# Performance work log

Measured on AMD Instinct MI355X. Metric: run time of the kernel, lower is better.

## Reference

```python
import jax, jax.numpy as jnp
import numpy as np

NUM_HEADS = 16


def setup_inputs() -> dict:
    key = jax.random.key(0)
    k1, k2, k3 = jax.random.split(key, 3)
    B, N, C = 8, 1024, 1024
    x = jax.random.normal(k1, (B, N, C), dtype=jnp.float32)
    w_qkv = jax.random.normal(k2, (3 * C, C), dtype=jnp.float32) * (C ** -0.5)
    w_proj = jax.random.normal(k3, (C, C), dtype=jnp.float32) * (C ** -0.5)
    b_proj = jnp.zeros((C,), dtype=jnp.float32)
    return {"x": x, "w_qkv": w_qkv, "w_proj": w_proj, "b_proj": b_proj}


def reference(x, w_qkv, w_proj, b_proj):
    B, N, C = x.shape
    H = NUM_HEADS
    d = C // H
    scale = d ** -0.5
    # qkv projection: (B, N, 3C) -> (3, B, H, N, d)
    qkv = jnp.einsum('bnc,oc->bno', x, w_qkv)
    qkv = qkv.reshape(B, N, 3, H, d).transpose(2, 0, 3, 1, 4)
    q, k, v = qkv[0], qkv[1], qkv[2]
    # spatial attention
    attn = jnp.einsum('bhnd,bhmd->bhnm', q, k) * scale
    attn = jax.nn.softmax(attn, axis=-1)
    out = jnp.einsum('bhnm,bhmd->bhnd', attn, v)
    out = out.transpose(0, 2, 1, 3).reshape(B, N, C)
    # output projection
    return jnp.einsum('bnc,oc->bno', out, w_proj) + b_proj
```

## Files before the change

kernel.cpp:

```cpp
#include <hip/hip_runtime.h>
#include <hip/hip_bf16.h>

typedef unsigned short u16;
typedef unsigned int u32;
typedef __bf16 bf16x8 __attribute__((ext_vector_type(8)));
typedef float f32x4 __attribute__((ext_vector_type(4)));

__device__ __forceinline__ u16 f2b(float f) {
    __bf16 h = (__bf16)f;
    return __builtin_bit_cast(u16, h);
}
__device__ __forceinline__ u32 f2b2(float lo, float hi) {
    return (u32)f2b(lo) | ((u32)f2b(hi) << 16);
}
__device__ __forceinline__ f32x4 mfma16(bf16x8 a, bf16x8 b, f32x4 c) {
    return __builtin_amdgcn_mfma_f32_16x16x32_bf16(a, b, c, 0, 0, 0);
}
__device__ __forceinline__ void async16(const u16* gsrc, u16* ldst) {
    __builtin_amdgcn_global_load_lds(
        (const __attribute__((address_space(1))) void*)gsrc,
        (__attribute__((address_space(3))) void*)ldst, 16, 0, 0);
}

__global__ __launch_bounds__(256) void cvt_all(const float* __restrict__ x,
                                               const float* __restrict__ wq,
                                               const float* __restrict__ wp,
                                               u16* __restrict__ xb,
                                               u16* __restrict__ wqb,
                                               u16* __restrict__ wpb) {
    int i = (blockIdx.x * 256 + threadIdx.x) * 4;
    const float* src; u16* dst; int off;
    if (i < 8388608)       { src = x;  dst = xb;  off = i; }
    else if (i < 11534336) { src = wq; dst = wqb; off = i - 8388608; }
    else                   { src = wp; dst = wpb; off = i - 11534336; }
    float4 f = *(const float4*)(src + off);
    ushort4 o;
    o.x = f2b(f.x); o.y = f2b(f.y); o.z = f2b(f.z); o.w = f2b(f.w);
    *(ushort4*)(dst + off) = o;
}

template <bool F32OUT>
__device__ __forceinline__ void gemm_core(const u16* __restrict__ A,
                                          const u16* __restrict__ B,
                                          void* __restrict__ Cptr,
                                          const float* __restrict__ bias,
                                          int N, int K, int bm, int bn,
                                          u16* As, u16* Bs) {
    const int tid  = threadIdx.x;
    const int lane = tid & 63, wid = tid >> 6;
    const int quad = lane >> 4, l16 = lane & 15;
    const int wm = (wid >> 1) * 64, wn = (wid & 1) * 64;
    const int srow = tid >> 2;
    const int scol = (tid & 3) * 8;

    const u16* Abase = A + (size_t)(bm * 128) * K + scol;
    const u16* Bbase = B + (size_t)(bn * 128) * K + scol;

    f32x4 acc[4][4] = {};

    for (int k0 = 0; k0 < K; k0 += 32) {
        __syncthreads();
        async16(Abase + (size_t)srow * K + k0,        &As[wid * 512]);
        async16(Abase + (size_t)(64 + srow) * K + k0, &As[2048 + wid * 512]);
        async16(Bbase + (size_t)srow * K + k0,        &Bs[wid * 512]);
        async16(Bbase + (size_t)(64 + srow) * K + k0, &Bs[2048 + wid * 512]);
        __syncthreads();
        bf16x8 af[4], bfr[4];
#pragma unroll
        for (int mt = 0; mt < 4; mt++)
            af[mt] = *(const bf16x8*)&As[(wm + mt * 16 + l16) * 32 + quad * 8];
#pragma unroll
        for (int nt = 0; nt < 4; nt++)
            bfr[nt] = *(const bf16x8*)&Bs[(wn + nt * 16 + l16) * 32 + quad * 8];
#pragma unroll
        for (int mt = 0; mt < 4; mt++)
#pragma unroll
            for (int nt = 0; nt < 4; nt++)
                acc[mt][nt] = mfma16(af[mt], bfr[nt], acc[mt][nt]);
    }
#pragma unroll
    for (int mt = 0; mt < 4; mt++) {
#pragma unroll
        for (int nt = 0; nt < 4; nt++) {
            int row = bm * 128 + wm + mt * 16 + quad * 4;
            int col = bn * 128 + wn + nt * 16 + l16;
            float bv = F32OUT ? bias[col] : 0.f;
#pragma unroll
            for (int r = 0; r < 4; r++) {
                if (F32OUT)
                    ((float*)Cptr)[(size_t)(row + r) * N + col] = acc[mt][nt][r] + bv;
                else
                    ((u16*)Cptr)[(size_t)(row + r) * N + col] = f2b(acc[mt][nt][r]);
            }
        }
    }
}

__global__ __launch_bounds__(256) void gemm_qkvt(const u16* __restrict__ xb,
                                                 const u16* __restrict__ wqkvb,
                                                 u16* __restrict__ qkb,
                                                 u16* __restrict__ vTb) {
    __shared__ u16 As[128 * 32];
    __shared__ u16 Bs[128 * 32];
    int id = blockIdx.x;
    if (id < 1024) {
        gemm_core<false>(xb, wqkvb, qkb, nullptr, 2048, 1024, id >> 4, id & 15, As, Bs);
    } else {
        int t = id - 1024;
        gemm_core<false>(wqkvb + (size_t)2048 * 1024, xb, vTb, nullptr,
                         8192, 1024, t >> 6, t & 63, As, Bs);
    }
}

__global__ __launch_bounds__(256) void gemm_proj(const u16* __restrict__ A,
                                                 const u16* __restrict__ B,
                                                 void* __restrict__ C,
                                                 const float* __restrict__ bias) {
    __shared__ u16 As[128 * 32];
    __shared__ u16 Bs[128 * 32];
    gemm_core<true>(A, B, C, bias, 1024, 1024, blockIdx.y, blockIdx.x, As, Bs);
}

__global__ __launch_bounds__(256, 4) void attn_kernel(const u16* __restrict__ qk,
                                                      const u16* __restrict__ vT,
                                                      u16* __restrict__ outb) {
    __shared__ u16 Qs[64 * 64];
    __shared__ u16 Ks[64 * 64];
    __shared__ u16 Vt[64 * 64];
    __shared__ u16 Ps[4 * 16 * 72];
    const int tid = threadIdx.x, lane = tid & 63, wid = tid >> 6;
    const int quad = lane >> 4, l16 = lane & 15;
    const int qt = blockIdx.x;
    const int bh = blockIdx.y;
    const int b = bh >> 4, h = bh & 15;
    const size_t base = (size_t)b * 1024;
    const int hoff = h * 64;
    const float CEXP = 0.125f * 1.44269504f;

    const int sr_ = lane >> 3;
    const int sc_ = ((lane & 7) ^ sr_) * 8;
    const int sw = l16 & 7;

#pragma unroll
    for (int j = 0; j < 2; ++j) {
        int rg = wid * 16 + j * 8;
        async16(qk + (base + qt * 64 + rg + sr_) * 2048 + hoff + sc_, &Qs[rg * 64]);
    }

    f32x4 Oacc[4] = {};
    float lp[4] = {0.f, 0.f, 0.f, 0.f};
    bf16x8 bq[2];
    u16* Pw = &Ps[wid * (16 * 72)];

    for (int kt = 0; kt < 16; ++kt) {
        __syncthreads();
#pragma unroll
        for (int j = 0; j < 2; ++j) {
            int rg = wid * 16 + j * 8;
            async16(qk + (base + kt * 64 + rg + sr_) * 2048 + 1024 + hoff + sc_,
                    &Ks[rg * 64]);
            async16(vT + (size_t)(hoff + rg + sr_) * 8192 + base + kt * 64 + sc_,
                    &Vt[rg * 64]);
        }
        __syncthreads();

        if (kt == 0) {
            int row = wid * 16 + l16;
            bq[0] = *(const bf16x8*)&Qs[row * 64 + ((quad ^ sw) << 3)];
            bq[1] = *(const bf16x8*)&Qs[row * 64 + (((4 + quad) ^ sw) << 3)];
        }

        f32x4 sacc[4] = {};
#pragma unroll
        for (int nt = 0; nt < 4; nt++) {
            int row = nt * 16 + l16;
            bf16x8 ak0 = *(const bf16x8*)&Ks[row * 64 + ((quad ^ sw) << 3)];
            bf16x8 ak1 = *(const bf16x8*)&Ks[row * 64 + (((4 + quad) ^ sw) << 3)];
            sacc[nt] = mfma16(ak0, bq[0], sacc[nt]);
            sacc[nt] = mfma16(ak1, bq[1], sacc[nt]);
        }

#pragma unroll
        for (int nt = 0; nt < 4; nt++) {
            float p0 = exp2f(sacc[nt][0] * CEXP);
            float p1 = exp2f(sacc[nt][1] * CEXP);
            float p2 = exp2f(sacc[nt][2] * CEXP);
            float p3 = exp2f(sacc[nt][3] * CEXP);
            lp[0] += p0; lp[1] += p1; lp[2] += p2; lp[3] += p3;
            uint2 pk; pk.x = f2b2(p0, p1); pk.y = f2b2(p2, p3);
            *(uint2*)&Pw[l16 * 72 + nt * 16 + quad * 4] = pk;
        }

        asm volatile("s_waitcnt lgkmcnt(0)" ::: "memory");
        __builtin_amdgcn_wave_barrier();

#pragma unroll
        for (int kc = 0; kc < 2; kc++) {
            bf16x8 ap = *(const bf16x8*)&Pw[l16 * 72 + kc * 32 + quad * 8];
#pragma unroll
            for (int nv = 0; nv < 4; nv++) {
                int row = nv * 16 + l16;
                bf16x8 bv = *(const bf16x8*)&Vt[row * 64 + (((kc * 4 + quad) ^ sw) << 3)];
                Oacc[nv] = mfma16(ap, bv, Oacc[nv]);
            }
        }
    }

    float l = (lp[0] + lp[1]) + (lp[2] + lp[3]);
    l += __shfl_xor(l, 16);
    l += __shfl_xor(l, 32);
    float inv[4];
#pragma unroll
    for (int r = 0; r < 4; r++) inv[r] = 1.f / __shfl(l, quad * 4 + r);

#pragma unroll
    for (int nv = 0; nv < 4; nv++)
#pragma unroll
        for (int r = 0; r < 4; r++) {
            int row = qt * 64 + wid * 16 + quad * 4 + r;
            int col = hoff + nv * 16 + l16;
            outb[(base + row) * 1024 + col] = f2b(Oacc[nv][r] * inv[r]);
        }
}

extern "C" void kernel_launch(void* const* d_in, const int* in_sizes, int n_in,
                              void* d_out, int out_size, void* d_ws, size_t ws_size,
                              hipStream_t stream) {
    const float* x      = (const float*)d_in[0];
    const float* w_qkv  = (const float*)d_in[1];
    const float* w_proj = (const float*)d_in[2];
    const float* b_proj = (const float*)d_in[3];

    char* ws = (char*)d_ws;
    u16* xb     = (u16*)(ws);
    u16* wqkvb  = (u16*)(ws + 16777216);
    u16* wprojb = (u16*)(ws + 23068672);
    u16* qkb    = (u16*)(ws + 25165824);
    u16* vTb    = (u16*)(ws + 58720256);
    u16* attnb  = (u16*)(ws + 75497472);

    cvt_all<<<12288, 256, 0, stream>>>(x, w_qkv, w_proj, xb, wqkvb, wprojb);
    gemm_qkvt<<<1536, 256, 0, stream>>>(xb, wqkvb, qkb, vTb);
    attn_kernel<<<dim3(16, 128), 256, 0, stream>>>(qkb, vTb, attnb);
    gemm_proj<<<dim3(8, 64), 256, 0, stream>>>(attnb, wprojb, d_out, b_proj);
}
```

Measured before the change: 252.5 us.

## Double-buffer K/V tiles in attention, fold softmax scale into Q weights

The attention kernel now double-buffers K and V tiles in LDS, prefetching the next tile while computing the current one, so each iteration needs one load-wait instead of a full load-then-compute serialization. Q is loaded straight from global into registers, dropping the Q LDS stage. The softmax scale times log2(e) is folded into the Q rows of the bf16 weight conversion, removing a multiply per score. Row sums are computed with an extra MFMA against a ones vector instead of per-lane adds and shuffles, and the P buffer uses an XOR swizzle rather than padding. Folding the scale into bf16 weights slightly changes rounding, and softmax still has no max subtraction.

```diff
diff --git a/kernel.cpp b/kernel.cpp
--- a/kernel.cpp
+++ b/kernel.cpp
@@ -29,13 +29,15 @@
                                                u16* __restrict__ wqb,
                                                u16* __restrict__ wpb) {
     int i = (blockIdx.x * 256 + threadIdx.x) * 4;
-    const float* src; u16* dst; int off;
-    if (i < 8388608)       { src = x;  dst = xb;  off = i; }
-    else if (i < 11534336) { src = wq; dst = wqb; off = i - 8388608; }
-    else                   { src = wp; dst = wpb; off = i - 11534336; }
+    const float* src; u16* dst; int off; float scl;
+    if (i < 8388608)       { src = x;  dst = xb;  off = i;            scl = 1.f; }
+    else if (i < 9437184)  { src = wq; dst = wqb; off = i - 8388608;  scl = 0.18033688f; }
+    else if (i < 11534336) { src = wq; dst = wqb; off = i - 8388608;  scl = 1.f; }
+    else                   { src = wp; dst = wpb; off = i - 11534336; scl = 1.f; }
     float4 f = *(const float4*)(src + off);
     ushort4 o;
-    o.x = f2b(f.x); o.y = f2b(f.y); o.z = f2b(f.z); o.w = f2b(f.w);
+    o.x = f2b(f.x * scl); o.y = f2b(f.y * scl);
+    o.z = f2b(f.z * scl); o.w = f2b(f.w * scl);
     *(ushort4*)(dst + off) = o;
 }
 
@@ -124,10 +126,9 @@
 __global__ __launch_bounds__(256, 4) void attn_kernel(const u16* __restrict__ qk,
                                                       const u16* __restrict__ vT,
                                                       u16* __restrict__ outb) {
-    __shared__ u16 Qs[64 * 64];
-    __shared__ u16 Ks[64 * 64];
-    __shared__ u16 Vt[64 * 64];
-    __shared__ u16 Ps[4 * 16 * 72];
+    __shared__ u16 Ks[2][64 * 64];
+    __shared__ u16 Vt[2][64 * 64];
+    __shared__ u16 Ps[4 * 16 * 64];
     const int tid = threadIdx.x, lane = tid & 63, wid = tid >> 6;
     const int quad = lane >> 4, l16 = lane & 15;
     const int qt = blockIdx.x;
@@ -135,83 +136,87 @@
     const int b = bh >> 4, h = bh & 15;
     const size_t base = (size_t)b * 1024;
     const int hoff = h * 64;
-    const float CEXP = 0.125f * 1.44269504f;
 
     const int sr_ = lane >> 3;
     const int sc_ = ((lane & 7) ^ sr_) * 8;
     const int sw = l16 & 7;
 
-#pragma unroll
-    for (int j = 0; j < 2; ++j) {
-        int rg = wid * 16 + j * 8;
-        async16(qk + (base + qt * 64 + rg + sr_) * 2048 + hoff + sc_, &Qs[rg * 64]);
-    }
-
-    f32x4 Oacc[4] = {};
-    float lp[4] = {0.f, 0.f, 0.f, 0.f};
-    bf16x8 bq[2];
-    u16* Pw = &Ps[wid * (16 * 72)];
-
-    for (int kt = 0; kt < 16; ++kt) {
-        __syncthreads();
+    const u16* qptr = qk + (base + qt * 64 + wid * 16 + l16) * 2048 + hoff + quad * 8;
+    bf16x8 bq0 = *(const bf16x8*)qptr;
+    bf16x8 bq1 = *(const bf16x8*)(qptr + 32);
+
+    auto stage = [&](int kt, int bs) {
 #pragma unroll
         for (int j = 0; j < 2; ++j) {
             int rg = wid * 16 + j * 8;
             async16(qk + (base + kt * 64 + rg + sr_) * 2048 + 1024 + hoff + sc_,
-                    &Ks[rg * 64]);
+                    &Ks[bs][rg * 64]);
             async16(vT + (size_t)(hoff + rg + sr_) * 8192 + base + kt * 64 + sc_,
-                    &Vt[rg * 64]);
-        }
-        __syncthreads();
-
-        if (kt == 0) {
-            int row = wid * 16 + l16;
-            bq[0] = *(const bf16x8*)&Qs[row * 64 + ((quad ^ sw) << 3)];
-            bq[1] = *(const bf16x8*)&Qs[row * 64 + (((4 + quad) ^ sw) << 3)];
-        }
+                    &Vt[bs][rg * 64]);
+        }
+    };
+    stage(0, 0);
+
+    f32x4 Oacc[4] = {};
+    f32x4 lacc = {};
+    bf16x8 vone;
+#pragma unroll
+    for (int i = 0; i < 8; ++i) vone[i] = (__bf16)1.0f;
+    u16* Pw = &Ps[wid * (16 * 64)];
+
+    for (int t = 0; t < 16; ++t) {
+        const int cur = t & 1;
+        __builtin_amdgcn_s_barrier();
+        __builtin_amdgcn_sched_barrier(0);
+        if (t < 15) {
+            stage(t + 1, cur ^ 1);
+            asm volatile("s_waitcnt vmcnt(4)" ::: "memory");
+        } else {
+            asm volatile("s_waitcnt vmcnt(0)" ::: "memory");
+        }
+        __builtin_amdgcn_s_barrier();
+        __builtin_amdgcn_sched_barrier(0);
 
         f32x4 sacc[4] = {};
 #pragma unroll
         for (int nt = 0; nt < 4; nt++) {
             int row = nt * 16 + l16;
-            bf16x8 ak0 = *(const bf16x8*)&Ks[row * 64 + ((quad ^ sw) << 3)];
-            bf16x8 ak1 = *(const bf16x8*)&Ks[row * 64 + (((4 + quad) ^ sw) << 3)];
-            sacc[nt] = mfma16(ak0, bq[0], sacc[nt]);
-            sacc[nt] = mfma16(ak1, bq[1], sacc[nt]);
+            bf16x8 ak0 = *(const bf16x8*)&Ks[cur][row * 64 + ((quad ^ sw) << 3)];
+            bf16x8 ak1 = *(const bf16x8*)&Ks[cur][row * 64 + (((4 + quad) ^ sw) << 3)];
+            sacc[nt] = mfma16(ak0, bq0, sacc[nt]);
+            sacc[nt] = mfma16(ak1, bq1, sacc[nt]);
         }
 
 #pragma unroll
         for (int nt = 0; nt < 4; nt++) {
-            float p0 = exp2f(sacc[nt][0] * CEXP);
-            float p1 = exp2f(sacc[nt][1] * CEXP);
-            float p2 = exp2f(sacc[nt][2] * CEXP);
-            float p3 = exp2f(sacc[nt][3] * CEXP);
-            lp[0] += p0; lp[1] += p1; lp[2] += p2; lp[3] += p3;
+            float p0 = exp2f(sacc[nt][0]);
+            float p1 = exp2f(sacc[nt][1]);
+            float p2 = exp2f(sacc[nt][2]);
+            float p3 = exp2f(sacc[nt][3]);
             uint2 pk; pk.x = f2b2(p0, p1); pk.y = f2b2(p2, p3);
-            *(uint2*)&Pw[l16 * 72 + nt * 16 + quad * 4] = pk;
+            *(uint2*)&Pw[l16 * 64 + (((nt * 2 + (quad >> 1)) ^ sw) << 3) + ((quad & 1) << 2)] = pk;
         }
 
         asm volatile("s_waitcnt lgkmcnt(0)" ::: "memory");
         __builtin_amdgcn_wave_barrier();
+        __builtin_amdgcn_sched_barrier(0);
 
 #pragma unroll
         for (int kc = 0; kc < 2; kc++) {
-            bf16x8 ap = *(const bf16x8*)&Pw[l16 * 72 + kc * 32 + quad * 8];
+            bf16x8 ap = *(const bf16x8*)&Pw[l16 * 64 + (((kc * 4 + quad) ^ sw) << 3)];
+            lacc = mfma16(ap, vone, lacc);
 #pragma unroll
             for (int nv = 0; nv < 4; nv++) {
                 int row = nv * 16 + l16;
-                bf16x8 bv = *(const bf16x8*)&Vt[row * 64 + (((kc * 4 + quad) ^ sw) << 3)];
+                bf16x8 bv = *(const bf16x8*)&Vt[cur][row * 64 + (((kc * 4 + quad) ^ sw) << 3)];
                 Oacc[nv] = mfma16(ap, bv, Oacc[nv]);
             }
         }
     }
 
-    float l = (lp[0] + lp[1]) + (lp[2] + lp[3]);
-    l += __shfl_xor(l, 16);
-    l += __shfl_xor(l, 32);
     float inv[4];
 #pragma unroll
-    for (int r = 0; r < 4; r++) inv[r] = 1.f / __shfl(l, quad * 4 + r);
+    for (int r = 0; r < 4; r++) inv[r] = 1.f / lacc[r];
 
 #pragma unroll
     for (int nv = 0; nv < 4; nv++)
```

New measurement: 247.6 us. Within noise of the previous version (-1.9%).
